# Performance work log

Hardware: AMD Instinct MI355X
Metric: run time of the kernel (lower is better)

Reference implementation:

```python
import jax, jax.numpy as jnp
import numpy as np

B, S, D = 8, 1024, 1024      # batch, seq_len, inp_dim
H, HD = 8, 64                # head_num, head_dim
HID = H * HD                 # hidden_dim = 512
P = 2 * D                    # p_factor * inp_dim = 2048
K = 4                        # causal conv kernel size
EPS = 1e-6
CAP = 15.0                   # soft cap for i/f gates


def _layernorm(x, g, b):
    mu = jnp.mean(x, -1, keepdims=True)
    var = jnp.var(x, -1, keepdims=True)
    return (x - mu) * jax.lax.rsqrt(var + EPS) * g + b


def _soft_cap(v):
    return CAP * jnp.tanh(v / CAP)


def _causal_conv_feat(x, w, b):
    # Conv1d(1,1,K) applied over the FEATURE axis of each timestep (as in the
    # torch code: x_t.unsqueeze(1) -> (bs,1,P)), causal left pad of K-1.
    L = x.shape[-1]
    xp = jnp.pad(x, ((0, 0), (0, 0), (K - 1, 0)))
    out = b
    for m in range(K):
        out = out + w[m] * xp[..., m:m + L]
    return out


def _forward(x, ln_g, ln_b, mh_g, mh_b, W_up_l, b_up_l, W_up_r, b_up_r,
             W_down, b_down, conv_w, conv_b, W_skip, b_skip, W_i, b_i,
             W_f, b_f, W_o, b_o, W_q, b_q, W_k, b_k, W_v, b_v):
    Bs, Sl, _ = x.shape
    xn = _layernorm(x, ln_g, ln_b)
    x_t = xn @ W_up_l.T + b_up_l                      # (B,S,P)
    r_t = xn @ W_up_r.T + b_up_r                      # (B,S,HID)
    x_c = jax.nn.silu(_causal_conv_feat(x_t, conv_w, conv_b))
    x_skip = x_c @ W_skip.T + b_skip                  # (B,S,HID)
    q = (x_c @ W_q.T + b_q).reshape(Bs, Sl, H, HD)
    k = (x_c @ W_k.T + b_k).reshape(Bs, Sl, H, HD) / float(np.sqrt(HD))
    v = (x_t @ W_v.T + b_v).reshape(Bs, Sl, H, HD)
    i_pre = _soft_cap(x_c @ W_i.T + b_i)              # (B,S,H)
    f_pre = _soft_cap(x_c @ W_f.T + b_f)              # (B,S,H)
    o = jax.nn.sigmoid(x_t @ W_o.T + b_o)             # (B,S,HID)

    def step(carry, inp):
        c, n, m = carry
        qt, kt, vt, it, ft = inp
        m_t = jnp.maximum(ft + m, it)
        ie = jnp.exp(it - m_t)
        fe = jnp.exp(ft - m_t + m)
        c = fe[:, :, None, None] * c + ie[:, :, None, None] * jnp.einsum('bhd,bhe->bhde', vt, kt)
        n = fe[:, :, None] * n + ie[:, :, None] * kt
        num = jnp.einsum('bhde,bhe->bhd', c, qt)
        den = jnp.maximum(jnp.sum(n * qt, -1, keepdims=True), 1.0)
        return (c, n, m_t), num / den

    c0 = jnp.zeros((Bs, H, HD, HD), x.dtype)
    n0 = jnp.ones((Bs, H, HD), x.dtype)
    m0 = jnp.zeros((Bs, H), x.dtype)
    seq = tuple(jnp.moveaxis(a, 1, 0) for a in (q, k, v, i_pre, f_pre))
    _, hs = jax.lax.scan(step, (c0, n0, m0), seq)     # hs: (S,B,H,HD)
    h = o * jnp.moveaxis(hs, 0, 1).reshape(Bs, Sl, HID)
    hn = _layernorm(h.reshape(Bs, Sl, H, HD), mh_g, mh_b).reshape(Bs, Sl, HID)
    out = (hn + x_skip) * jax.nn.silu(r_t)
    return out @ W_down.T + b_down + x


def setup_inputs() -> dict:
    key = jax.random.key(0)
    ks = jax.random.split(key, 16)

    def w(kk, shape):
        return jax.random.normal(kk, shape, jnp.float32) / np.sqrt(shape[-1]).astype(np.float32)

    return {
        'x': jax.random.normal(ks[0], (B, S, D), jnp.float32),
        'ln_g': jnp.ones((D,), jnp.float32), 'ln_b': jnp.zeros((D,), jnp.float32),
        'mh_g': jnp.ones((H, HD), jnp.float32), 'mh_b': jnp.zeros((H, HD), jnp.float32),
        'W_up_l': w(ks[1], (P, D)), 'b_up_l': jnp.zeros((P,), jnp.float32),
        'W_up_r': w(ks[2], (HID, D)), 'b_up_r': jnp.zeros((HID,), jnp.float32),
        'W_down': w(ks[3], (D, HID)), 'b_down': jnp.zeros((D,), jnp.float32),
        'conv_w': jax.random.normal(ks[4], (K,), jnp.float32) * 0.3,
        'conv_b': jnp.zeros((), jnp.float32),
        'W_skip': w(ks[5], (HID, P)), 'b_skip': jnp.zeros((HID,), jnp.float32),
        'W_i': w(ks[6], (H, P)), 'b_i': jnp.zeros((H,), jnp.float32),
        'W_f': w(ks[7], (H, P)), 'b_f': jnp.zeros((H,), jnp.float32),
        'W_o': w(ks[8], (HID, P)), 'b_o': jnp.zeros((HID,), jnp.float32),
        'W_q': w(ks[9], (HID, P)), 'b_q': jnp.zeros((HID,), jnp.float32),
        'W_k': w(ks[10], (HID, P)), 'b_k': jnp.zeros((HID,), jnp.float32),
        'W_v': w(ks[11], (HID, P)), 'b_v': jnp.zeros((HID,), jnp.float32),
    }


def reference(x, ln_g, ln_b, mh_g, mh_b, W_up_l, b_up_l, W_up_r, b_up_r,
              W_down, b_down, conv_w, conv_b, W_skip, b_skip, W_i, b_i,
              W_f, b_f, W_o, b_o, W_q, b_q, W_k, b_k, W_v, b_v):
    return _forward(x, ln_g, ln_b, mh_g, mh_b, W_up_l, b_up_l, W_up_r, b_up_r,
                    W_down, b_down, conv_w, conv_b, W_skip, b_skip, W_i, b_i,
                    W_f, b_f, W_o, b_o, W_q, b_q, W_k, b_k, W_v, b_v)
```

## Files before the change

### kernel.cpp

```cpp
#include <hip/hip_runtime.h>
#include <hip/hip_bf16.h>
#include <math.h>

#define Bq 8
#define Sq 1024
#define Dq 1024
#define Hq 8
#define HDq 64
#define HIDq 512
#define Pq 2048
#define EPSq 1e-6f
#define CAPq 15.0f
#define NCq 16
#define CLq 64
#define LDST 40
#define ARENA (128 * LDST)
#define GEMM_SMEM_BYTES (2 * 4 * ARENA * 2)

typedef __attribute__((ext_vector_type(8))) short short8;
typedef __attribute__((ext_vector_type(4))) float f32x4v;
typedef __hip_bfloat16 bf16;

__device__ inline void split2(float v, bf16& h, bf16& l) {
  h = __float2bfloat16(v);
  l = __float2bfloat16(v - __bfloat162float(h));
}

__global__ __launch_bounds__(256) void cvtw_all(
    const float* __restrict__ s0, const float* __restrict__ s1,
    const float* __restrict__ s2, const float* __restrict__ s3,
    const float* __restrict__ s4, const float* __restrict__ s5,
    const float* __restrict__ s6, const float* __restrict__ s7,
    bf16* __restrict__ hi, bf16* __restrict__ lo)
{
  int u = blockIdx.x * 256 + threadIdx.x;
  const float* src; int segBase;
  if      (u <  524288) { src = s0; segBase = 0;       }
  else if (u <  655360) { src = s1; segBase = 524288;  }
  else if (u <  917504) { src = s2; segBase = 655360;  }
  else if (u < 1179648) { src = s3; segBase = 917504;  }
  else if (u < 1441792) { src = s4; segBase = 1179648; }
  else if (u < 1703936) { src = s5; segBase = 1441792; }
  else if (u < 1966080) { src = s6; segBase = 1703936; }
  else                  { src = s7; segBase = 1966080; }
  float4 v = ((const float4*)src)[u - segBase];
  size_t o = (size_t)u * 4;
  bf16 h, l;
  split2(v.x, h, l); hi[o+0] = h; lo[o+0] = l;
  split2(v.y, h, l); hi[o+1] = h; lo[o+1] = l;
  split2(v.z, h, l); hi[o+2] = h; lo[o+2] = l;
  split2(v.w, h, l); hi[o+3] = h; lo[o+3] = l;
}

__global__ __launch_bounds__(256) void ln_kernel(const float* __restrict__ x,
    const float* __restrict__ g, const float* __restrict__ b,
    bf16* __restrict__ yh, bf16* __restrict__ yl)
{
  int row = blockIdx.x;
  int tid = threadIdx.x;
  const float* xr = x + (size_t)row * Dq;
  float v[4]; float s = 0.f, s2 = 0.f;
  #pragma unroll
  for (int i = 0; i < 4; i++) { v[i] = xr[tid + 256*i]; s += v[i]; s2 += v[i]*v[i]; }
  #pragma unroll
  for (int mm = 32; mm > 0; mm >>= 1) { s += __shfl_xor(s, mm, 64); s2 += __shfl_xor(s2, mm, 64); }
  __shared__ float rs[4], rs2[4];
  int lane = tid & 63, wave = tid >> 6;
  if (lane == 0) { rs[wave] = s; rs2[wave] = s2; }
  __syncthreads();
  s  = rs[0] + rs[1] + rs[2] + rs[3];
  s2 = rs2[0] + rs2[1] + rs2[2] + rs2[3];
  float mu  = s * (1.f / Dq);
  float var = s2 * (1.f / Dq) - mu * mu;
  float r = rsqrtf(var + EPSq);
  #pragma unroll
  for (int i = 0; i < 4; i++) {
    int c = tid + 256*i;
    float y = (v[i] - mu) * r * g[c] + b[c];
    bf16 h, l; split2(y, h, l);
    yh[(size_t)row * Dq + c] = h;
    yl[(size_t)row * Dq + c] = l;
  }
}

__global__ __launch_bounds__(256) void gemm_x3(
    const bf16* __restrict__ Ahi, const bf16* __restrict__ Alo,
    const bf16* __restrict__ Whi, const bf16* __restrict__ Wlo,
    int Kd, int start1, int start2, const float* __restrict__ resid,
    const float* bias0, float* f0, bf16* h0, bf16* l0, int w0, float sc0, int a0,
    const float* bias1, float* f1, bf16* h1, bf16* l1, int w1, float sc1, int a1,
    const float* bias2, float* f2, bf16* h2, bf16* l2, int w2, float sc2, int a2)
{
  extern __shared__ short smem[];
  int tid = threadIdx.x;
  int lane = tid & 63, wave = tid >> 6;
  int wr = wave >> 1, wc = wave & 1;
  int rowBase = blockIdx.y * 128;
  int colBase = blockIdx.x * 128;

  int sk  = (tid & 3) * 8;
  int sr0 = tid >> 2;
  int sr1 = 64 + sr0;

  const short* Ahg = (const short*)Ahi + (size_t)rowBase * Kd;
  const short* Alg = (const short*)Alo + (size_t)rowBase * Kd;
  const short* Bhg = (const short*)Whi + (size_t)colBase * Kd;
  const short* Blg = (const short*)Wlo + (size_t)colBase * Kd;

  f32x4v acc[4][4];
  #pragma unroll
  for (int i = 0; i < 4; i++)
    #pragma unroll
    for (int j = 0; j < 4; j++) acc[i][j] = (f32x4v){0.f, 0.f, 0.f, 0.f};

  int fk = (lane >> 4) * 8;
  int fr = lane & 15;
  int nk = Kd >> 5;

  short8 ah0, ah1, al0, al1, bh0, bh1, bl0, bl1;

#define LOAD_TILE(k0) do {                                                    \
    size_t o0 = (size_t)sr0 * Kd + (k0) + sk;                                 \
    size_t o1 = (size_t)sr1 * Kd + (k0) + sk;                                 \
    ah0 = *(const short8*)(Ahg + o0); ah1 = *(const short8*)(Ahg + o1);       \
    al0 = *(const short8*)(Alg + o0); al1 = *(const short8*)(Alg + o1);       \
    bh0 = *(const short8*)(Bhg + o0); bh1 = *(const short8*)(Bhg + o1);       \
    bl0 = *(const short8*)(Blg + o0); bl1 = *(const short8*)(Blg + o1);       \
  } while (0)

#define STORE_TILE(S) do {                                                    \
    *(short8*)&(S)[0*ARENA + sr0*LDST + sk] = ah0;                            \
    *(short8*)&(S)[0*ARENA + sr1*LDST + sk] = ah1;                            \
    *(short8*)&(S)[1*ARENA + sr0*LDST + sk] = al0;                            \
    *(short8*)&(S)[1*ARENA + sr1*LDST + sk] = al1;                            \
    *(short8*)&(S)[2*ARENA + sr0*LDST + sk] = bh0;                            \
    *(short8*)&(S)[2*ARENA + sr1*LDST + sk] = bh1;                            \
    *(short8*)&(S)[3*ARENA + sr0*LDST + sk] = bl0;                            \
    *(short8*)&(S)[3*ARENA + sr1*LDST + sk] = bl1;                            \
  } while (0)

  LOAD_TILE(0);
  STORE_TILE(smem);
  __syncthreads();

  for (int t = 0; t < nk; ++t) {
    const short* C = smem + (t & 1) * (4 * ARENA);
    short* Nx      = smem + ((t + 1) & 1) * (4 * ARENA);
    bool pf = (t + 1 < nk);
    if (pf) LOAD_TILE((size_t)(t + 1) << 5);

    short8 afh[4], afl[4], bfh[4], bfl[4];
    #pragma unroll
    for (int mi = 0; mi < 4; mi++) {
      afh[mi] = *(const short8*)&C[0*ARENA + (wr * 64 + mi * 16 + fr) * LDST + fk];
      afl[mi] = *(const short8*)&C[1*ARENA + (wr * 64 + mi * 16 + fr) * LDST + fk];
    }
    #pragma unroll
    for (int ni = 0; ni < 4; ni++) {
      bfh[ni] = *(const short8*)&C[2*ARENA + (wc * 64 + ni * 16 + fr) * LDST + fk];
      bfl[ni] = *(const short8*)&C[3*ARENA + (wc * 64 + ni * 16 + fr) * LDST + fk];
    }
    #pragma unroll
    for (int mi = 0; mi < 4; mi++)
      #pragma unroll
      for (int ni = 0; ni < 4; ni++)
        acc[mi][ni] = __builtin_amdgcn_mfma_f32_16x16x32_bf16(afh[mi], bfh[ni], acc[mi][ni], 0, 0, 0);
    #pragma unroll
    for (int mi = 0; mi < 4; mi++)
      #pragma unroll
      for (int ni = 0; ni < 4; ni++)
        acc[mi][ni] = __builtin_amdgcn_mfma_f32_16x16x32_bf16(afh[mi], bfl[ni], acc[mi][ni], 0, 0, 0);
    #pragma unroll
    for (int mi = 0; mi < 4; mi++)
      #pragma unroll
      for (int ni = 0; ni < 4; ni++)
        acc[mi][ni] = __builtin_amdgcn_mfma_f32_16x16x32_bf16(afl[mi], bfh[ni], acc[mi][ni], 0, 0, 0);

    __builtin_amdgcn_sched_barrier(0);
    if (pf) STORE_TILE(Nx);
    __syncthreads();
  }
#undef LOAD_TILE
#undef STORE_TILE

  const float* bias; float* fOut; bf16* hOut; bf16* lOut; int segStart, segW; float sscale; int sact;
  if (colBase >= start2)      { bias=bias2; fOut=f2; hOut=h2; lOut=l2; segStart=start2; segW=w2; sscale=sc2; sact=a2; }
  else if (colBase >= start1) { bias=bias1; fOut=f1; hOut=h1; lOut=l1; segStart=start1; segW=w1; sscale=sc1; sact=a1; }
  else                        { bias=bias0; fOut=f0; hOut=h0; lOut=l0; segStart=0;      segW=w0; sscale=sc0; sact=a0; }

  int cr = (lane >> 4) * 4;
  int cc = lane & 15;
  #pragma unroll
  for (int mi = 0; mi < 4; mi++) {
    #pragma unroll
    for (int ni = 0; ni < 4; ni++) {
      int col  = colBase + wc * 64 + ni * 16 + cc;
      int colL = col - segStart;
      float bv = bias[colL];
      #pragma unroll
      for (int j = 0; j < 4; j++) {
        int row = rowBase + wr * 64 + mi * 16 + cr + j;
        float val = (acc[mi][ni][j] + bv) * sscale;
        if (sact) val = 1.f / (1.f + expf(-val));
        if (resid && segStart == 0) val += resid[(size_t)row * segW + colL];
        size_t oidx = (size_t)row * segW + colL;
        if (fOut) fOut[oidx] = val;
        if (hOut) {
          bf16 h, l; split2(val, h, l);
          hOut[oidx] = h; lOut[oidx] = l;
        }
      }
    }
  }
}

__global__ __launch_bounds__(256) void conv_kernel(const bf16* __restrict__ xth,
    const bf16* __restrict__ xtl, const float* __restrict__ cw,
    const float* __restrict__ cb, bf16* __restrict__ xch, bf16* __restrict__ xcl,
    int total)
{
  int idx = blockIdx.x * 256 + threadIdx.x;
  if (idx >= total) return;
  int p = idx & (Pq - 1);
  #define XT(i) (__bfloat162float(xth[i]) + __bfloat162float(xtl[i]))
  float acc = cb[0] + cw[3] * XT(idx);
  if (p >= 1) acc += cw[2] * XT(idx - 1);
  if (p >= 2) acc += cw[1] * XT(idx - 2);
  if (p >= 3) acc += cw[0] * XT(idx - 3);
  #undef XT
  float y = acc / (1.f + expf(-acc));
  bf16 h, l; split2(y, h, l);
  xch[idx] = h; xcl[idx] = l;
}

__global__ __launch_bounds__(256) void ifk_kernel(const bf16* __restrict__ xch,
    const bf16* __restrict__ xcl,
    const float* __restrict__ Wi, const float* __restrict__ bi,
    const float* __restrict__ Wf, const float* __restrict__ bf_,
    float* __restrict__ ip, float* __restrict__ fp)
{
  int row = blockIdx.x;
  int lane = threadIdx.x & 63, wave = threadIdx.x >> 6;
  size_t rb = (size_t)row * Pq;
  for (int oi = wave; oi < 16; oi += 4) {
    int hh = oi & 7;
    const float* Wrow = (oi < 8) ? (Wi + (size_t)hh * Pq) : (Wf + (size_t)hh * Pq);
    float s = 0.f;
    for (int j = lane; j < Pq; j += 64)
      s += (__bfloat162float(xch[rb + j]) + __bfloat162float(xcl[rb + j])) * Wrow[j];
    #pragma unroll
    for (int mm = 32; mm > 0; mm >>= 1) s += __shfl_xor(s, mm, 64);
    if (lane == 0) {
      float val = s + ((oi < 8) ? bi[hh] : bf_[hh]);
      val = CAPq * tanhf(val / CAPq);
      if (oi < 8) ip[(size_t)row * Hq + hh] = val;
      else        fp[(size_t)row * Hq + hh] = val;
    }
  }
}

__global__ __launch_bounds__(256) void chunkA_kernel(const float* __restrict__ k,
    const float* __restrict__ v, const float* __restrict__ ip,
    const float* __restrict__ fp, float* __restrict__ bg,
    float* __restrict__ FcMc, float* __restrict__ kvg, float* __restrict__ ksumg)
{
  int blk = blockIdx.x;
  int bh = blk >> 4, c = blk & 15;
  int b = bh >> 3, hh = bh & 7;
  int tid = threadIdx.x, lane = tid & 63, wave = tid >> 6;

  __shared__ float sK[64][64], sV[64][64], sW[64];

  size_t base = (size_t)b * Sq * 512 + (size_t)hh * 64 + (size_t)c * CLq * 512;
  #pragma unroll 4
  for (int i = 0; i < 16; i++) {
    int t = wave * 16 + i;
    sK[t][lane] = k[base + (size_t)t * 512 + lane];
    sV[t][lane] = v[base + (size_t)t * 512 + lane];
  }
  if (tid < 64) {
    size_t ifb = ((size_t)b * Sq + c * CLq + tid) * Hq + hh;
    float fv = fp[ifb], iv = ip[ifb];
    float cf = fv;
    #pragma unroll
    for (int off = 1; off < 64; off <<= 1) {
      float t2 = __shfl_up(cf, off, 64);
      if (lane >= off) cf += t2;
    }
    float bs = iv - cf;
    float mx = bs;
    #pragma unroll
    for (int off = 1; off < 64; off <<= 1) {
      float t2 = __shfl_up(mx, off, 64);
      if (lane >= off) mx = fmaxf(mx, t2);
    }
    float Mc = __shfl(mx, 63, 64);
    bg[(size_t)blk * 64 + tid] = bs;
    sW[tid] = expf(bs - Mc);
    if (tid == 63) { FcMc[blk*2] = cf; FcMc[blk*2+1] = Mc; }
  }
  __syncthreads();
  float acc[16];
  #pragma unroll
  for (int j = 0; j < 16; j++) acc[j] = 0.f;
  for (int s = 0; s < 64; s++) {
    float wv = sW[s] * sV[s][lane];
    #pragma unroll
    for (int j = 0; j < 16; j++) acc[j] += wv * sK[s][wave*16+j];
  }
  float* kvp = kvg + (size_t)blk * 4096 + lane * 64 + wave * 16;
  #pragma unroll
  for (int j = 0; j < 16; j++) kvp[j] = acc[j];
  if (tid < 64) {
    float a = 0.f;
    for (int s = 0; s < 64; s++) a += sW[s] * sK[s][tid];
    ksumg[(size_t)blk * 64 + tid] = a;
  }
}

__global__ __launch_bounds__(256) void chunkB_kernel(const float* __restrict__ kvg,
    const float* __restrict__ ksumg, const float* __restrict__ FcMc,
    float* __restrict__ boundC, float* __restrict__ boundN, float* __restrict__ boundM)
{
  int bh = blockIdx.x;
  int tid = threadIdx.x, lane = tid & 63, wave = tid >> 6;
  float C[16];
  #pragma unroll
  for (int j = 0; j < 16; j++) C[j] = 0.f;
  float ne = 1.0f, m = 0.f;
  for (int c = 0; c < NCq; c++) {
    size_t blk = (size_t)bh * NCq + c;
    float* bC = boundC + blk * 4096 + lane * 64 + wave * 16;
    #pragma unroll
    for (int j = 0; j < 16; j++) bC[j] = C[j];
    if (wave == 0) boundN[blk * 64 + lane] = ne;
    if (tid == 0)  boundM[blk] = m;
    float Fc = FcMc[blk * 2], Mc = FcMc[blk * 2 + 1];
    float mm = fmaxf(m, Mc);
    float a1 = expf(m - mm), a2 = expf(Mc - mm);
    const float* kv = kvg + blk * 4096 + lane * 64 + wave * 16;
    #pragma unroll
    for (int j = 0; j < 16; j++) C[j] = a1 * C[j] + a2 * kv[j];
    ne = a1 * ne + a2 * ksumg[blk * 64 + lane];
    m = Fc + mm;
  }
}

__global__ __launch_bounds__(256) void chunkC_kernel(const float* q,
    const float* __restrict__ k, const float* __restrict__ v,
    const float* __restrict__ bg, const float* __restrict__ boundC,
    const float* __restrict__ boundN, const float* __restrict__ boundM,
    float* hs)
{
  int blk = blockIdx.x;
  int bh = blk >> 4, c = blk & 15;
  int b = bh >> 3, hh = bh & 7;
  int tid = threadIdx.x, lane = tid & 63, wave = tid >> 6;

  __shared__ float sQ[64][65], sKV[64][65], sS[64][65];
  __shared__ float sB[64], sMr[64], sNin[64];

  size_t base = (size_t)b * Sq * 512 + (size_t)hh * 64 + (size_t)c * CLq * 512;
  #pragma unroll 4
  for (int i = 0; i < 16; i++) {
    int t = wave * 16 + i;
    sQ[t][lane]  = q[base + (size_t)t * 512 + lane];
    sKV[t][lane] = k[base + (size_t)t * 512 + lane];
  }
  float m_in = boundM[blk];
  if (tid < 64) {
    float bs = bg[(size_t)blk * 64 + tid];
    float mx = bs;
    #pragma unroll
    for (int off = 1; off < 64; off <<= 1) {
      float t2 = __shfl_up(mx, off, 64);
      if (lane >= off) mx = fmaxf(mx, t2);
    }
    sB[tid]   = bs;
    sMr[tid]  = fmaxf(m_in, mx);
    sNin[tid] = boundN[(size_t)blk * 64 + tid];
  }
  __syncthreads();

  {
    int t = lane;
    float acc[16];
    #pragma unroll
    for (int j = 0; j < 16; j++) acc[j] = 0.f;
    for (int d = 0; d < 64; d++) {
      float qv = sQ[t][d];
      #pragma unroll
      for (int j = 0; j < 16; j++) acc[j] += qv * sKV[wave*16+j][d];
    }
    float Mr = sMr[t];
    #pragma unroll
    for (int j = 0; j < 16; j++) {
      int s = wave * 16 + j;
      float w = (s <= t) ? expf(sB[s] - Mr) : 0.f;
      sS[t][s] = w * acc[j];
    }
  }
  __syncthreads();
  #pragma unroll 4
  for (int i = 0; i < 16; i++) {
    int t = wave * 16 + i;
    sKV[t][lane] = v[base + (size_t)t * 512 + lane];
  }
  __syncthreads();

  {
    int t = lane;
    float Mr = sMr[t];
    float bfac = expf(m_in - Mr);
    float den = 0.f;
    for (int d = 0; d < 64; d++) den += sNin[d] * sQ[t][d];
    den *= bfac;
    float num[16];
    #pragma unroll
    for (int j = 0; j < 16; j++) num[j] = 0.f;
    const float* Crow = boundC + (size_t)blk * 4096;
    for (int e = 0; e < 64; e++) {
      float qv = sQ[t][e];
      #pragma unroll
      for (int j = 0; j < 16; j++)
        num[j] += Crow[(size_t)(wave*16+j) * 64 + e] * qv;
    }
    #pragma unroll
    for (int j = 0; j < 16; j++) num[j] *= bfac;
    for (int s = 0; s < 64; s++) {
      float ws = sS[t][s];
      den += ws;
      #pragma unroll
      for (int j = 0; j < 16; j++) num[j] += ws * sKV[s][wave*16+j];
    }
    den = fmaxf(den, 1.0f);
    float o[16];
    #pragma unroll
    for (int j = 0; j < 16; j++) o[j] = num[j] / den;
    float* hp = hs + base + (size_t)t * 512 + wave * 16;
    #pragma unroll
    for (int j4 = 0; j4 < 4; j4++)
      ((float4*)hp)[j4] = ((float4*)o)[j4];
  }
}

__global__ __launch_bounds__(256) void epi_kernel(const float* __restrict__ hsv,
    const float* __restrict__ ov, const float* __restrict__ xs,
    const float* __restrict__ rt, const float* __restrict__ mg,
    const float* __restrict__ mb, bf16* __restrict__ pdh, bf16* __restrict__ pdl)
{
  int tid = threadIdx.x;
  int lane = tid & 63, wave = tid >> 6;
  size_t row = (size_t)blockIdx.x * 4 + wave;
  int hh = (int)(row & 7);
  size_t idx = row * 64 + lane;
  float hv = ov[idx] * hsv[idx];
  float s = hv, s2 = hv * hv;
  #pragma unroll
  for (int mm = 32; mm > 0; mm >>= 1) { s += __shfl_xor(s, mm, 64); s2 += __shfl_xor(s2, mm, 64); }
  float mu  = s * (1.f / 64.f);
  float var = s2 * (1.f / 64.f) - mu * mu;
  float r = rsqrtf(var + EPSq);
  float hn = (hv - mu) * r * mg[hh * 64 + lane] + mb[hh * 64 + lane];
  float rv = rt[idx];
  float y = (hn + xs[idx]) * (rv / (1.f + expf(-rv)));
  bf16 h, l; split2(y, h, l);
  pdh[idx] = h; pdl[idx] = l;
}

extern "C" void kernel_launch(void* const* d_in, const int* in_sizes, int n_in,
                              void* d_out, int out_size, void* d_ws, size_t ws_size,
                              hipStream_t stream)
{
  const float* x      = (const float*)d_in[0];
  const float* ln_g   = (const float*)d_in[1];
  const float* ln_b   = (const float*)d_in[2];
  const float* mh_g   = (const float*)d_in[3];
  const float* mh_b   = (const float*)d_in[4];
  const float* W_up_l = (const float*)d_in[5];
  const float* b_up_l = (const float*)d_in[6];
  const float* W_up_r = (const float*)d_in[7];
  const float* b_up_r = (const float*)d_in[8];
  const float* W_down = (const float*)d_in[9];
  const float* b_down = (const float*)d_in[10];
  const float* conv_w = (const float*)d_in[11];
  const float* conv_b = (const float*)d_in[12];
  const float* W_skip = (const float*)d_in[13];
  const float* b_skip = (const float*)d_in[14];
  const float* W_i    = (const float*)d_in[15];
  const float* b_i    = (const float*)d_in[16];
  const float* W_f    = (const float*)d_in[17];
  const float* b_f    = (const float*)d_in[18];
  const float* W_o    = (const float*)d_in[19];
  const float* b_o    = (const float*)d_in[20];
  const float* W_q    = (const float*)d_in[21];
  const float* b_q    = (const float*)d_in[22];
  const float* W_k    = (const float*)d_in[23];
  const float* b_k    = (const float*)d_in[24];
  const float* W_v    = (const float*)d_in[25];
  const float* b_v    = (const float*)d_in[26];
  float* out = (float*)d_out;

  const size_t MB = 1u << 20;
  if (ws_size < 193 * MB) return;

  static bool attrSet = false;
  if (!attrSet) {
    (void)hipFuncSetAttribute(reinterpret_cast<const void*>(gemm_x3),
                              hipFuncAttributeMaxDynamicSharedMemorySize,
                              GEMM_SMEM_BYTES);
    attrSet = true;
  }

  char* base = (char*)d_ws;
  bf16* whi = (bf16*)base;
  bf16* wlo = (bf16*)(base + 16*MB);
  bf16* xnh = (bf16*)(base + 32*MB);
  bf16* xnl = (bf16*)(base + 48*MB);
  bf16* xth = (bf16*)(base + 64*MB);
  bf16* xtl = (bf16*)(base + 96*MB);
  bf16* xch = (bf16*)(base + 128*MB);
  bf16* xcl = (bf16*)(base + 160*MB);
  float* vb  = (float*)(base + 32*MB);
  float* ob  = (float*)(base + 48*MB);
  float* xs  = (float*)(base + 64*MB);
  float* qb  = (float*)(base + 80*MB);
  float* kb  = (float*)(base + 96*MB);
  bf16*  pdh = (bf16*)(base + 112*MB);
  bf16*  pdl = (bf16*)(base + 120*MB);
  float* kvg    = (float*)(base + 128*MB);
  float* boundC = (float*)(base + 144*MB);
  float* bg     = (float*)(base + 160*MB);
  float* ksumg  = (float*)(base + 160*MB + 256*1024);
  float* boundN = (float*)(base + 160*MB + 512*1024);
  float* FcMc   = (float*)(base + 160*MB + 768*1024);
  float* boundM = (float*)(base + 160*MB + 776*1024);
  float* ip  = (float*)(base + 192*MB);
  float* fpb = (float*)(base + 192*MB + 256*1024);
  float* rt  = out;
  float* hsb = qb;

  const int Mrows = Bq * Sq;
  const int BIG = 1 << 30;

  cvtw_all<<<dim3(8192), dim3(256), 0, stream>>>(
      W_up_l, W_up_r, W_v, W_o, W_skip, W_q, W_k, W_down, whi, wlo);

  ln_kernel<<<dim3(Mrows), dim3(256), 0, stream>>>(x, ln_g, ln_b, xnh, xnl);

  gemm_x3<<<dim3(20, 64), dim3(256), GEMM_SMEM_BYTES, stream>>>(
      xnh, xnl, whi, wlo, 1024, 2048, BIG, nullptr,
      b_up_l, nullptr, xth, xtl, 2048, 1.f, 0,
      b_up_r, rt, nullptr, nullptr, 512, 1.f, 0,
      nullptr, nullptr, nullptr, nullptr, 1, 1.f, 0);

  gemm_x3<<<dim3(8, 64), dim3(256), GEMM_SMEM_BYTES, stream>>>(
      xth, xtl, whi + 2621440, wlo + 2621440, 2048, 512, BIG, nullptr,
      b_v, vb, nullptr, nullptr, 512, 1.f, 0,
      b_o, ob, nullptr, nullptr, 512, 1.f, 1,
      nullptr, nullptr, nullptr, nullptr, 1, 1.f, 0);

  int convTotal = Mrows * Pq;
  conv_kernel<<<dim3(convTotal / 256), dim3(256), 0, stream>>>(
      xth, xtl, conv_w, conv_b, xch, xcl, convTotal);

  gemm_x3<<<dim3(12, 64), dim3(256), GEMM_SMEM_BYTES, stream>>>(
      xch, xcl, whi + 4718592, wlo + 4718592, 2048, 512, 1024, nullptr,
      b_skip, xs, nullptr, nullptr, 512, 1.f, 0,
      b_q, qb, nullptr, nullptr, 512, 1.f, 0,
      b_k, kb, nullptr, nullptr, 512, 0.125f, 0);

  ifk_kernel<<<dim3(Mrows), dim3(256), 0, stream>>>(
      xch, xcl, W_i, b_i, W_f, b_f, ip, fpb);

  chunkA_kernel<<<dim3(Bq * Hq * NCq), dim3(256), 0, stream>>>(
      kb, vb, ip, fpb, bg, FcMc, kvg, ksumg);
  chunkB_kernel<<<dim3(Bq * Hq), dim3(256), 0, stream>>>(
      kvg, ksumg, FcMc, boundC, boundN, boundM);
  chunkC_kernel<<<dim3(Bq * Hq * NCq), dim3(256), 0, stream>>>(
      qb, kb, vb, bg, boundC, boundN, boundM, hsb);

  epi_kernel<<<dim3(Mrows * Hq / 4), dim3(256), 0, stream>>>(
      hsb, ob, xs, rt, mh_g, mh_b, pdh, pdl);

  gemm_x3<<<dim3(8, 64), dim3(256), GEMM_SMEM_BYTES, stream>>>(
      pdh, pdl, whi + 7864320, wlo + 7864320, 512, BIG, BIG, x,
      b_down, out, nullptr, nullptr, 1024, 1.f, 0,
      nullptr, nullptr, nullptr, nullptr, 1, 1.f, 0,
      nullptr, nullptr, nullptr, nullptr, 1, 1.f, 0);
}
```

Baseline: 1.005 ms.

## Deepen GEMM prefetch to two register stages and remap blocks across XCDs

Restructures the split-bf16 GEMM main loop to keep two register-staged tiles in flight, loading tile t+2 while computing tile t. The loop is manually unrolled by two, and full __syncthreads is replaced with an LDS waitcnt plus s_barrier. It also remaps the flat block index so consecutive blocks land on the same XCD chunk (8-way interleave), aiming at better L2 locality. Costs are more VGPR pressure from the second staging set, and the loop assumes an even number of K tiles and a block count divisible by 8.

```diff
diff --git a/kernel.cpp b/kernel.cpp
--- a/kernel.cpp
+++ b/kernel.cpp
@@ -83,6 +83,64 @@
   }
 }
 
+struct Stage { short8 ah0, ah1, al0, al1, bh0, bh1, bl0, bl1; };
+
+__device__ __forceinline__ void load_tile(Stage& st,
+    const short* Ahg, const short* Alg, const short* Bhg, const short* Blg,
+    int Kd, int sr0, int sr1, int sk, int k0)
+{
+  size_t o0 = (size_t)sr0 * Kd + k0 + sk;
+  size_t o1 = (size_t)sr1 * Kd + k0 + sk;
+  st.ah0 = *(const short8*)(Ahg + o0); st.ah1 = *(const short8*)(Ahg + o1);
+  st.al0 = *(const short8*)(Alg + o0); st.al1 = *(const short8*)(Alg + o1);
+  st.bh0 = *(const short8*)(Bhg + o0); st.bh1 = *(const short8*)(Bhg + o1);
+  st.bl0 = *(const short8*)(Blg + o0); st.bl1 = *(const short8*)(Blg + o1);
+}
+
+__device__ __forceinline__ void store_tile(short* S, const Stage& st,
+                                           int sr0, int sr1, int sk)
+{
+  *(short8*)&S[0*ARENA + sr0*LDST + sk] = st.ah0;
+  *(short8*)&S[0*ARENA + sr1*LDST + sk] = st.ah1;
+  *(short8*)&S[1*ARENA + sr0*LDST + sk] = st.al0;
+  *(short8*)&S[1*ARENA + sr1*LDST + sk] = st.al1;
+  *(short8*)&S[2*ARENA + sr0*LDST + sk] = st.bh0;
+  *(short8*)&S[2*ARENA + sr1*LDST + sk] = st.bh1;
+  *(short8*)&S[3*ARENA + sr0*LDST + sk] = st.bl0;
+  *(short8*)&S[3*ARENA + sr1*LDST + sk] = st.bl1;
+}
+
+__device__ __forceinline__ void frag_mfma(const short* C, int wr, int wc,
+                                          int fr, int fk, f32x4v acc[4][4])
+{
+  short8 afh[4], afl[4], bfh[4], bfl[4];
+  #pragma unroll
+  for (int mi = 0; mi < 4; mi++) {
+    afh[mi] = *(const short8*)&C[0*ARENA + (wr * 64 + mi * 16 + fr) * LDST + fk];
+    afl[mi] = *(const short8*)&C[1*ARENA + (wr * 64 + mi * 16 + fr) * LDST + fk];
+  }
+  #pragma unroll
+  for (int ni = 0; ni < 4; ni++) {
+    bfh[ni] = *(const short8*)&C[2*ARENA + (wc * 64 + ni * 16 + fr) * LDST + fk];
+    bfl[ni] = *(const short8*)&C[3*ARENA + (wc * 64 + ni * 16 + fr) * LDST + fk];
+  }
+  #pragma unroll
+  for (int mi = 0; mi < 4; mi++)
+    #pragma unroll
+    for (int ni = 0; ni < 4; ni++)
+      acc[mi][ni] = __builtin_amdgcn_mfma_f32_16x16x32_bf16(afh[mi], bfh[ni], acc[mi][ni], 0, 0, 0);
+  #pragma unroll
+  for (int mi = 0; mi < 4; mi++)
+    #pragma unroll
+    for (int ni = 0; ni < 4; ni++)
+      acc[mi][ni] = __builtin_amdgcn_mfma_f32_16x16x32_bf16(afh[mi], bfl[ni], acc[mi][ni], 0, 0, 0);
+  #pragma unroll
+  for (int mi = 0; mi < 4; mi++)
+    #pragma unroll
+    for (int ni = 0; ni < 4; ni++)
+      acc[mi][ni] = __builtin_amdgcn_mfma_f32_16x16x32_bf16(afl[mi], bfh[ni], acc[mi][ni], 0, 0, 0);
+}
+
 __global__ __launch_bounds__(256) void gemm_x3(
     const bf16* __restrict__ Ahi, const bf16* __restrict__ Alo,
     const bf16* __restrict__ Whi, const bf16* __restrict__ Wlo,
@@ -95,8 +153,15 @@
   int tid = threadIdx.x;
   int lane = tid & 63, wave = tid >> 6;
   int wr = wave >> 1, wc = wave & 1;
-  int rowBase = blockIdx.y * 128;
-  int colBase = blockIdx.x * 128;
+
+  int gx = gridDim.x;
+  int flat = blockIdx.y * gx + blockIdx.x;
+  int nb = gx * gridDim.y;
+  int chunk = nb >> 3;
+  int nid = (flat & 7) * chunk + (flat >> 3);
+  int col = nid % gx, row = nid / gx;
+  int rowBase = row * 128;
+  int colBase = col * 128;
 
   int sk  = (tid & 3) * 8;
   int sr0 = tid >> 2;
@@ -117,71 +182,35 @@
   int fr = lane & 15;
   int nk = Kd >> 5;
 
-  short8 ah0, ah1, al0, al1, bh0, bh1, bl0, bl1;
-
-#define LOAD_TILE(k0) do {                                                    \
-    size_t o0 = (size_t)sr0 * Kd + (k0) + sk;                                 \
-    size_t o1 = (size_t)sr1 * Kd + (k0) + sk;                                 \
-    ah0 = *(const short8*)(Ahg + o0); ah1 = *(const short8*)(Ahg + o1);       \
-    al0 = *(const short8*)(Alg + o0); al1 = *(const short8*)(Alg + o1);       \
-    bh0 = *(const short8*)(Bhg + o0); bh1 = *(const short8*)(Bhg + o1);       \
-    bl0 = *(const short8*)(Blg + o0); bl1 = *(const short8*)(Blg + o1);       \
-  } while (0)
-
-#define STORE_TILE(S) do {                                                    \
-    *(short8*)&(S)[0*ARENA + sr0*LDST + sk] = ah0;                            \
-    *(short8*)&(S)[0*ARENA + sr1*LDST + sk] = ah1;                            \
-    *(short8*)&(S)[1*ARENA + sr0*LDST + sk] = al0;                            \
-    *(short8*)&(S)[1*ARENA + sr1*LDST + sk] = al1;                            \
-    *(short8*)&(S)[2*ARENA + sr0*LDST + sk] = bh0;                            \
-    *(short8*)&(S)[2*ARENA + sr1*LDST + sk] = bh1;                            \
-    *(short8*)&(S)[3*ARENA + sr0*LDST + sk] = bl0;                            \
-    *(short8*)&(S)[3*ARENA + sr1*LDST + sk] = bl1;                            \
-  } while (0)
-
-  LOAD_TILE(0);
-  STORE_TILE(smem);
-  __syncthreads();
-
-  for (int t = 0; t < nk; ++t) {
-    const short* C = smem + (t & 1) * (4 * ARENA);
-    short* Nx      = smem + ((t + 1) & 1) * (4 * ARENA);
-    bool pf = (t + 1 < nk);
-    if (pf) LOAD_TILE((size_t)(t + 1) << 5);
-
-    short8 afh[4], afl[4], bfh[4], bfl[4];
-    #pragma unroll
-    for (int mi = 0; mi < 4; mi++) {
-      afh[mi] = *(const short8*)&C[0*ARENA + (wr * 64 + mi * 16 + fr) * LDST + fk];
-      afl[mi] = *(const short8*)&C[1*ARENA + (wr * 64 + mi * 16 + fr) * LDST + fk];
-    }
-    #pragma unroll
-    for (int ni = 0; ni < 4; ni++) {
-      bfh[ni] = *(const short8*)&C[2*ARENA + (wc * 64 + ni * 16 + fr) * LDST + fk];
-      bfl[ni] = *(const short8*)&C[3*ARENA + (wc * 64 + ni * 16 + fr) * LDST + fk];
-    }
-    #pragma unroll
-    for (int mi = 0; mi < 4; mi++)
-      #pragma unroll
-      for (int ni = 0; ni < 4; ni++)
-        acc[mi][ni] = __builtin_amdgcn_mfma_f32_16x16x32_bf16(afh[mi], bfh[ni], acc[mi][ni], 0, 0, 0);
-    #pragma unroll
-    for (int mi = 0; mi < 4; mi++)
-      #pragma unroll
-      for (int ni = 0; ni < 4; ni++)
-        acc[mi][ni] = __builtin_amdgcn_mfma_f32_16x16x32_bf16(afh[mi], bfl[ni], acc[mi][ni], 0, 0, 0);
-    #pragma unroll
-    for (int mi = 0; mi < 4; mi++)
-      #pragma unroll
-      for (int ni = 0; ni < 4; ni++)
-        acc[mi][ni] = __builtin_amdgcn_mfma_f32_16x16x32_bf16(afl[mi], bfh[ni], acc[mi][ni], 0, 0, 0);
-
+  short* buf0 = smem;
+  short* buf1 = smem + 4 * ARENA;
+
+  Stage rgA, rgB;
+  load_tile(rgA, Ahg, Alg, Bhg, Blg, Kd, sr0, sr1, sk, 0);
+  load_tile(rgB, Ahg, Alg, Bhg, Blg, Kd, sr0, sr1, sk, 32);
+  store_tile(buf0, rgA, sr0, sr1, sk);
+  asm volatile("s_waitcnt lgkmcnt(0)" ::: "memory");
+  __builtin_amdgcn_s_barrier();
+
+  for (int t = 0; t < nk; t += 2) {
+    if (t + 2 < nk) load_tile(rgA, Ahg, Alg, Bhg, Blg, Kd, sr0, sr1, sk, (t + 2) * 32);
     __builtin_amdgcn_sched_barrier(0);
-    if (pf) STORE_TILE(Nx);
-    __syncthreads();
-  }
-#undef LOAD_TILE
-#undef STORE_TILE
+    frag_mfma(buf0, wr, wc, fr, fk, acc);
+    __builtin_amdgcn_sched_barrier(0);
+    store_tile(buf1, rgB, sr0, sr1, sk);
+    asm volatile("s_waitcnt lgkmcnt(0)" ::: "memory");
+    __builtin_amdgcn_s_barrier();
+
+    if (t + 3 < nk) load_tile(rgB, Ahg, Alg, Bhg, Blg, Kd, sr0, sr1, sk, (t + 3) * 32);
+    __builtin_amdgcn_sched_barrier(0);
+    frag_mfma(buf1, wr, wc, fr, fk, acc);
+    if (t + 2 < nk) {
+      __builtin_amdgcn_sched_barrier(0);
+      store_tile(buf0, rgA, sr0, sr1, sk);
+      asm volatile("s_waitcnt lgkmcnt(0)" ::: "memory");
+      __builtin_amdgcn_s_barrier();
+    }
+  }
 
   const float* bias; float* fOut; bf16* hOut; bf16* lOut; int segStart, segW; float sscale; int sact;
   if (colBase >= start2)      { bias=bias2; fOut=f2; hOut=h2; lOut=l2; segStart=start2; segW=w2; sscale=sc2; sact=a2; }
@@ -194,16 +223,16 @@
   for (int mi = 0; mi < 4; mi++) {
     #pragma unroll
     for (int ni = 0; ni < 4; ni++) {
-      int col  = colBase + wc * 64 + ni * 16 + cc;
-      int colL = col - segStart;
+      int colO  = colBase + wc * 64 + ni * 16 + cc;
+      int colL = colO - segStart;
       float bv = bias[colL];
       #pragma unroll
       for (int j = 0; j < 4; j++) {
-        int row = rowBase + wr * 64 + mi * 16 + cr + j;
+        int rowO = rowBase + wr * 64 + mi * 16 + cr + j;
         float val = (acc[mi][ni][j] + bv) * sscale;
         if (sact) val = 1.f / (1.f + expf(-val));
-        if (resid && segStart == 0) val += resid[(size_t)row * segW + colL];
-        size_t oidx = (size_t)row * segW + colL;
+        if (resid && segStart == 0) val += resid[(size_t)rowO * segW + colL];
+        size_t oidx = (size_t)rowO * segW + colL;
         if (fOut) fOut[oidx] = val;
         if (hOut) {
           bf16 h, l; split2(val, h, l);
```

After: 1.140 ms. +13.5%, slower.
